# Kernel optimization log

Hardware: AMD Instinct MI355X
Metric: run time of the kernel (lower is better)

The kernel has to match this reference:

```python
import jax, jax.numpy as jnp
import numpy as np

DIM_RGB = 400
DIM_POSE = 400
HIDDEN = 512
LN_EPS = 1e-5


def setup_inputs() -> dict:
    key = jax.random.key(0)
    ks = jax.random.split(key, 12)
    B, S_R, S_P = 32, 2048, 2048
    scale_in = 1.0 / np.sqrt(DIM_RGB)
    scale_h = 1.0 / np.sqrt(HIDDEN)
    return {
        "rgb": jax.random.normal(ks[0], (B, S_R, DIM_RGB), jnp.float32),
        "pose": jax.random.normal(ks[1], (B, S_P, DIM_POSE), jnp.float32),
        "Wq": jax.random.normal(ks[2], (DIM_RGB, HIDDEN), jnp.float32) * scale_in,
        "bq": jnp.zeros((HIDDEN,), jnp.float32),
        "Wk": jax.random.normal(ks[3], (DIM_POSE, HIDDEN), jnp.float32) * scale_in,
        "bk": jnp.zeros((HIDDEN,), jnp.float32),
        "Wv": jax.random.normal(ks[4], (DIM_POSE, HIDDEN), jnp.float32) * scale_in,
        "bv": jnp.zeros((HIDDEN,), jnp.float32),
        "Wp": jax.random.normal(ks[5], (HIDDEN, DIM_RGB), jnp.float32) * scale_h,
        "bp": jnp.zeros((DIM_RGB,), jnp.float32),
        "ln_gamma": jnp.ones((DIM_RGB,), jnp.float32),
        "ln_beta": jnp.zeros((DIM_RGB,), jnp.float32),
        "gate": jnp.ones((1,), jnp.float32),
    }


def reference(rgb, pose, Wq, bq, Wk, bk, Wv, bv, Wp, bp, ln_gamma, ln_beta, gate):
    # q: [B,Sr,H], k/v: [B,Sp,H]
    q = jnp.einsum("bsd,dh->bsh", rgb, Wq) + bq
    k = jnp.einsum("bsd,dh->bsh", pose, Wk) + bk
    v = jnp.einsum("bsd,dh->bsh", pose, Wv) + bv
    scores = jnp.einsum("bqh,bkh->bqk", q, k) / jnp.sqrt(jnp.asarray(HIDDEN, q.dtype))
    attn = jax.nn.softmax(scores, axis=-1)  # [B,Sr,Sp]
    out = jnp.einsum("bqk,bkh->bqh", attn, v)
    proj = jnp.einsum("bqh,hd->bqd", out, Wp) + bp
    x = rgb + gate * proj  # gated residual, gate broadcasts from shape (1,)
    mu = jnp.mean(x, axis=-1, keepdims=True)
    var = jnp.mean(jnp.square(x - mu), axis=-1, keepdims=True)
    fused = (x - mu) * jax.lax.rsqrt(var + LN_EPS) * ln_gamma + ln_beta
    return fused
```

## Files before the change

### kernel.cpp

```cpp
#include <hip/hip_runtime.h>
#include <stdint.h>

typedef unsigned short u16;
typedef unsigned int u32;
typedef __bf16 bf16x8 __attribute__((ext_vector_type(8)));
typedef float f32x4 __attribute__((ext_vector_type(4)));

#define S_LEN 2048
#define BATCH 32
#define DIM 400
#define HID 512
#define KPAD 448
#define MROWS (BATCH * S_LEN)
#define NB_CHUNK 8
#define SCALE_QK 0.04419417382415922f

__device__ __forceinline__ u16 f2bf(float f) {
  u32 u = __float_as_uint(f);
  u = u + 0x7fffu + ((u >> 16) & 1u);
  return (u16)(u >> 16);
}
__device__ __forceinline__ float bf2f(u16 h) {
  return __uint_as_float(((u32)h) << 16);
}

__device__ __forceinline__ void async_cp16(const void* gp, const void* lp) {
  __builtin_amdgcn_global_load_lds(
      (const __attribute__((address_space(1))) void*)gp,
      (__attribute__((address_space(3))) void*)(uintptr_t)lp,
      16, 0, 0);
}

template<int BN>
__global__ __launch_bounds__(512, 2)
void gemm256(const u16* __restrict__ A, const u16* __restrict__ B,
             u16* __restrict__ C, const float* __restrict__ bias,
             int K, int lda, int ldb, int ldc, int Nreal, float scale,
             long sA, long sB, long sC, int mode)
{
  constexpr int NJ   = (BN == 256) ? 4 : 2;
  constexpr int COLW = (BN == 256) ? 64 : 32;
  constexpr int ASZ  = 16384;
  constexpr int BSZ  = (BN == 256) ? 16384 : 8192;
  __shared__ __align__(16) u16 SM[2 * ASZ + 2 * BSZ];

#define ABUF(i) (&SM[0] + (i) * ASZ)
#define BBUF(i) (&SM[0] + 2 * ASZ + (i) * BSZ)

  const int tid = threadIdx.x;
  const int lane = tid & 63;
  const int w = tid >> 6;
  const int wm = w >> 2, wn = w & 3;

  int mt, nt, bz;
  if (mode == 1) {
    const int lin = (int)blockIdx.x + ((int)blockIdx.y << 8);
    const int c = lin & 7, j = lin >> 3;
    mt = c * 32 + (j >> 1); nt = j & 1; bz = 0;
  } else if (mode == 2) {
    bz = blockIdx.x; mt = blockIdx.y; nt = blockIdx.z;
  } else if (mode == 3) {
    bz = blockIdx.x; mt = blockIdx.z; nt = blockIdx.y;
  } else {
    mt = blockIdx.x; nt = blockIdx.y; bz = blockIdx.z;
  }
  const long m0 = (long)mt * 256;
  const long n0 = (long)nt * BN;
  const u16* Ab = A + (long)bz * sA;
  const u16* Bb = B + (long)bz * sB;
  u16* Cb = C + (long)bz * sC;
  const int T = K >> 6;

  const int sr = tid >> 3, si = tid & 7;
  const u16 *gA[2][2], *gB[2][2];
#pragma unroll
  for (int h = 0; h < 2; h++)
#pragma unroll
    for (int j = 0; j < 2; j++) {
      const int Ra = h * 128 + sr + j * 64;
      const int ka = si ^ ((Ra >> 1) & 7);
      gA[h][j] = Ab + (m0 + Ra) * (long)lda + ka * 8;
      const int Rb = ((BN == 256) ? h * 128 : 0) + sr + j * 64;
      const int kb = si ^ ((Rb >> 1) & 7);
      gB[h][j] = Bb + (n0 + Rb) * (long)ldb + kb * 8;
    }

#define ISS(g0, g1, kt, lp) { async_cp16((g0) + (kt), (lp) + tid * 8); \
                              async_cp16((g1) + (kt), (lp) + 4096 + tid * 8); }

  if constexpr (BN == 256) {
    ISS(gB[0][0], gB[0][1], 0,  BBUF(0));
    ISS(gB[1][0], gB[1][1], 0,  BBUF(0) + 8192);
    ISS(gA[0][0], gA[0][1], 0,  ABUF(0));
    ISS(gA[1][0], gA[1][1], 0,  ABUF(0) + 8192);
    ISS(gB[0][0], gB[0][1], 64, BBUF(1));
    ISS(gB[1][0], gB[1][1], 64, BBUF(1) + 8192);
    asm volatile("s_waitcnt vmcnt(4)" ::: "memory");
  } else {
    ISS(gB[0][0], gB[0][1], 0,  BBUF(0));
    ISS(gA[0][0], gA[0][1], 0,  ABUF(0));
    ISS(gA[1][0], gA[1][1], 0,  ABUF(0) + 8192);
    ISS(gB[0][0], gB[0][1], 64, BBUF(1));
    asm volatile("s_waitcnt vmcnt(2)" ::: "memory");
  }
  asm volatile("s_barrier" ::: "memory");

  f32x4 acc[8][NJ] = {};
  const int l15 = lane & 15, l4 = lane >> 4;

#define LDA(dst, ig) { const int R_ = wm * 128 + (ig) * 16 + l15; \
    const int sw_ = (R_ >> 1) & 7; \
    dst[0] = *(const bf16x8*)&Asc[R_ * 64 + ((l4) ^ sw_) * 8]; \
    dst[1] = *(const bf16x8*)&Asc[R_ * 64 + ((4 + l4) ^ sw_) * 8]; }
#define LDB(dst, jg) { const int R_ = wn * COLW + (jg) * 16 + l15; \
    const int sw_ = (R_ >> 1) & 7; \
    dst[0] = *(const bf16x8*)&Bsc[R_ * 64 + ((l4) ^ sw_) * 8]; \
    dst[1] = *(const bf16x8*)&Bsc[R_ * 64 + ((4 + l4) ^ sw_) * 8]; }

  for (int t = 0; t < T; t++) {
    const int cur = t & 1, nxt = cur ^ 1;
    const u16* Asc = ABUF(cur);
    const u16* Bsc = BBUF(cur);
    const int kt1 = (t + 1) << 6, kt2 = (t + 2) << 6;
    bf16x8 afr[4][2], bfr[NJ][2];

    if (t + 1 < T) ISS(gA[0][0], gA[0][1], kt1, ABUF(nxt));
    LDB(bfr[0], 0); LDB(bfr[1], 1);
    if constexpr (BN == 256) { LDA(afr[0], 0); LDA(afr[1], 1); LDA(afr[2], 2); LDA(afr[3], 3); }
    else                     { LDA(afr[0], 0); LDA(afr[1], 1); }
    asm volatile("s_barrier" ::: "memory");
    __builtin_amdgcn_s_setprio(1);
#pragma unroll
    for (int ks = 0; ks < 2; ks++) {
      if constexpr (BN == 256) {
#pragma unroll
        for (int i = 0; i < 4; i++)
#pragma unroll
          for (int j = 0; j < 2; j++)
            acc[i][j] = __builtin_amdgcn_mfma_f32_16x16x32_bf16(afr[i][ks], bfr[j][ks], acc[i][j], 0, 0, 0);
      } else {
#pragma unroll
        for (int i = 0; i < 2; i++)
#pragma unroll
          for (int j = 0; j < 2; j++)
            acc[i][j] = __builtin_amdgcn_mfma_f32_16x16x32_bf16(afr[i][ks], bfr[j][ks], acc[i][j], 0, 0, 0);
      }
    }
    __builtin_amdgcn_s_setprio(0);
    asm volatile("s_barrier" ::: "memory");

    if (t + 1 < T) ISS(gA[1][0], gA[1][1], kt1, ABUF(nxt) + 8192);
    if constexpr (BN == 256) { LDB(bfr[2], 2); LDB(bfr[3], 3); }
    else                     { LDA(afr[2], 2); LDA(afr[3], 3); }
    asm volatile("s_barrier" ::: "memory");
    __builtin_amdgcn_s_setprio(1);
#pragma unroll
    for (int ks = 0; ks < 2; ks++) {
      if constexpr (BN == 256) {
#pragma unroll
        for (int i = 0; i < 4; i++)
#pragma unroll
          for (int j = 2; j < 4; j++)
            acc[i][j] = __builtin_amdgcn_mfma_f32_16x16x32_bf16(afr[i][ks], bfr[j][ks], acc[i][j], 0, 0, 0);
      } else {
#pragma unroll
        for (int i = 2; i < 4; i++)
#pragma unroll
          for (int j = 0; j < 2; j++)
            acc[i][j] = __builtin_amdgcn_mfma_f32_16x16x32_bf16(afr[i][ks], bfr[j][ks], acc[i][j], 0, 0, 0);
      }
    }
    __builtin_amdgcn_s_setprio(0);
    asm volatile("s_barrier" ::: "memory");

    if (t + 2 < T) ISS(gB[0][0], gB[0][1], kt2, BBUF(cur));
    if constexpr (BN == 256) { LDA(afr[0], 4); LDA(afr[1], 5); LDA(afr[2], 6); LDA(afr[3], 7); }
    else                     { LDA(afr[0], 4); LDA(afr[1], 5); }
    asm volatile("s_barrier" ::: "memory");
    __builtin_amdgcn_s_setprio(1);
#pragma unroll
    for (int ks = 0; ks < 2; ks++) {
      if constexpr (BN == 256) {
#pragma unroll
        for (int i = 0; i < 4; i++)
#pragma unroll
          for (int j = 0; j < 2; j++)
            acc[4 + i][j] = __builtin_amdgcn_mfma_f32_16x16x32_bf16(afr[i][ks], bfr[j][ks], acc[4 + i][j], 0, 0, 0);
      } else {
#pragma unroll
        for (int i = 0; i < 2; i++)
#pragma unroll
          for (int j = 0; j < 2; j++)
            acc[4 + i][j] = __builtin_amdgcn_mfma_f32_16x16x32_bf16(afr[i][ks], bfr[j][ks], acc[4 + i][j], 0, 0, 0);
      }
    }
    __builtin_amdgcn_s_setprio(0);
    asm volatile("s_barrier" ::: "memory");

    if constexpr (BN == 256) {
      if (t + 2 < T) ISS(gB[1][0], gB[1][1], kt2, BBUF(cur) + 8192);
    } else {
      LDA(afr[2], 6); LDA(afr[3], 7);
    }
    asm volatile("s_barrier" ::: "memory");
    __builtin_amdgcn_s_setprio(1);
#pragma unroll
    for (int ks = 0; ks < 2; ks++) {
      if constexpr (BN == 256) {
#pragma unroll
        for (int i = 0; i < 4; i++)
#pragma unroll
          for (int j = 2; j < 4; j++)
            acc[4 + i][j] = __builtin_amdgcn_mfma_f32_16x16x32_bf16(afr[i][ks], bfr[j][ks], acc[4 + i][j], 0, 0, 0);
      } else {
#pragma unroll
        for (int i = 2; i < 4; i++)
#pragma unroll
          for (int j = 0; j < 2; j++)
            acc[4 + i][j] = __builtin_amdgcn_mfma_f32_16x16x32_bf16(afr[i][ks], bfr[j][ks], acc[4 + i][j], 0, 0, 0);
      }
    }
    __builtin_amdgcn_s_setprio(0);
    if (t < T - 2) {
      if constexpr (BN == 256) asm volatile("s_waitcnt vmcnt(4)" ::: "memory");
      else                     asm volatile("s_waitcnt vmcnt(2)" ::: "memory");
    } else if (t == T - 2) {
      asm volatile("s_waitcnt vmcnt(0)" ::: "memory");
    }
    asm volatile("s_barrier" ::: "memory");
  }

  {
    u16* Cst = &SM[0];
    constexpr int RB = BN * 2;
#pragma unroll
    for (int j = 0; j < NJ; j++) {
      const int col = wn * COLW + j * 16 + l15;
      const int gcol = (int)n0 + col;
      const float bv = (bias && gcol < Nreal) ? bias[gcol] : 0.0f;
#pragma unroll
      for (int i = 0; i < 8; i++) {
#pragma unroll
        for (int r = 0; r < 4; r++) {
          const int row = wm * 128 + i * 16 + l4 * 4 + r;
          const int cb = (col * 2) ^ (((row >> 2) & 3) << 5);
          *(u16*)((char*)Cst + row * RB + cb) = f2bf(acc[i][j][r] * scale + bv);
        }
      }
    }
    __syncthreads();
    constexpr int CH = RB / 16;
    constexpr int NC = 256 * CH / 512;
#pragma unroll
    for (int i = 0; i < NC; i++) {
      const int chunk = tid + i * 512;
      const int row = chunk / CH;
      const int qb_ = (chunk % CH) * 16;
      const int swz = ((row >> 2) & 3) << 5;
      uint4 val = *(const uint4*)((const char*)Cst + row * RB + (qb_ ^ swz));
      const int col = (int)n0 + qb_ / 2;
      if (col < Nreal)
        *(uint4*)(Cb + (m0 + row) * (long)ldc + col) = val;
    }
  }
#undef ISS
#undef LDA
#undef LDB
#undef ABUF
#undef BBUF
}

__global__ __launch_bounds__(256)
void transpose_hs(const u16* __restrict__ v, u16* __restrict__ vT)
{
  __shared__ u16 tile[64][66];
  const int b = blockIdx.z;
  const long s0 = (long)blockIdx.x * 64;
  const long h0 = (long)blockIdx.y * 64;
  const u16* vb = v + (long)b * S_LEN * HID;
  u16* vTb = vT + (long)b * HID * S_LEN;
  const int t = threadIdx.x;
  const int rr = t >> 3;
  const int cs = (t & 7) * 8;
#pragma unroll
  for (int p = 0; p < 2; p++) {
    const int r = p * 32 + rr;
    uint4 d = *(const uint4*)(vb + (s0 + r) * HID + h0 + cs);
    const u16* ds = (const u16*)&d;
#pragma unroll
    for (int j = 0; j < 8; j++) tile[r][cs + j] = ds[j];
  }
  __syncthreads();
#pragma unroll
  for (int p = 0; p < 2; p++) {
    const int hc = p * 32 + rr;
    __align__(16) u16 tmp[8];
#pragma unroll
    for (int j = 0; j < 8; j++) tmp[j] = tile[cs + j][hc];
    *(uint4*)(vTb + (h0 + hc) * S_LEN + s0 + cs) = *(const uint4*)tmp;
  }
}

__global__ __launch_bounds__(256)
void softmax_rows(u16* __restrict__ sc)
{
  const int w = threadIdx.x >> 6, lane = threadIdx.x & 63;
  const long row = (long)blockIdx.x * 4 + w;
  u16* p = sc + row * (long)S_LEN;

  uint4 d[4];
#pragma unroll
  for (int k = 0; k < 4; k++) d[k] = *(const uint4*)(p + (k * 64 + lane) * 8);

  float x[32];
  float mx = -3.0e38f;
#pragma unroll
  for (int k = 0; k < 4; k++) {
    const u16* ds = (const u16*)&d[k];
#pragma unroll
    for (int j = 0; j < 8; j++) { x[k * 8 + j] = bf2f(ds[j]); mx = fmaxf(mx, x[k * 8 + j]); }
  }
#pragma unroll
  for (int o = 32; o > 0; o >>= 1) mx = fmaxf(mx, __shfl_xor(mx, o, 64));

  float s = 0.f;
#pragma unroll
  for (int e = 0; e < 32; e++) { x[e] = __expf(x[e] - mx); s += x[e]; }
#pragma unroll
  for (int o = 32; o > 0; o >>= 1) s += __shfl_xor(s, o, 64);
  const float inv = 1.0f / s;

#pragma unroll
  for (int k = 0; k < 4; k++) {
    __align__(16) u16 outv[8];
#pragma unroll
    for (int j = 0; j < 8; j++) outv[j] = f2bf(x[k * 8 + j] * inv);
    *(uint4*)(p + (k * 64 + lane) * 8) = *(const uint4*)outv;
  }
}

__global__ __launch_bounds__(256)
void fuse_ln(const float* __restrict__ rgb, const u16* __restrict__ proj,
             const float* __restrict__ gatep, const float* __restrict__ gamma,
             const float* __restrict__ beta, float* __restrict__ out)
{
  const int w = threadIdx.x >> 6, lane = threadIdx.x & 63;
  const long row = (long)blockIdx.x * 4 + w;
  const float g = gatep[0];
  const float* rp = rgb + row * DIM;
  const u16* pp = proj + row * DIM;
  float* op = out + row * DIM;
  const int c = lane * 8;
  const bool act = (lane < 50);

  float x[8];
  float s = 0.f, q = 0.f;
  if (act) {
    float4 r0 = *(const float4*)(rp + c);
    float4 r1 = *(const float4*)(rp + c + 4);
    uint4 pv = *(const uint4*)(pp + c);
    const u16* pb = (const u16*)&pv;
    float rr[8] = {r0.x, r0.y, r0.z, r0.w, r1.x, r1.y, r1.z, r1.w};
#pragma unroll
    for (int j = 0; j < 8; j++) {
      x[j] = rr[j] + g * bf2f(pb[j]);
      s += x[j]; q += x[j] * x[j];
    }
  }
#pragma unroll
  for (int o = 32; o > 0; o >>= 1) { s += __shfl_xor(s, o, 64); q += __shfl_xor(q, o, 64); }
  const float mean = s * (1.0f / DIM);
  const float var = q * (1.0f / DIM) - mean * mean;
  const float rstd = rsqrtf(var + 1e-5f);
  if (act) {
    float4 ga0 = *(const float4*)(gamma + c);
    float4 ga1 = *(const float4*)(gamma + c + 4);
    float4 be0 = *(const float4*)(beta + c);
    float4 be1 = *(const float4*)(beta + c + 4);
    float4 o0, o1;
    o0.x = (x[0] - mean) * rstd * ga0.x + be0.x;
    o0.y = (x[1] - mean) * rstd * ga0.y + be0.y;
    o0.z = (x[2] - mean) * rstd * ga0.z + be0.z;
    o0.w = (x[3] - mean) * rstd * ga0.w + be0.w;
    o1.x = (x[4] - mean) * rstd * ga1.x + be1.x;
    o1.y = (x[5] - mean) * rstd * ga1.y + be1.y;
    o1.z = (x[6] - mean) * rstd * ga1.z + be1.z;
    o1.w = (x[7] - mean) * rstd * ga1.w + be1.w;
    *(float4*)(op + c) = o0;
    *(float4*)(op + c + 4) = o1;
  }
}

__global__ __launch_bounds__(256)
void cvt_pad(const float* __restrict__ src, u16* __restrict__ dst)
{
  const long g = (long)blockIdx.x * 256 + threadIdx.x;
  const long row = g / 56;
  const int cs = (int)(g % 56) * 8;
  __align__(16) u16 o[8];
  if (cs + 8 <= DIM) {
    float4 r0 = *(const float4*)(src + row * DIM + cs);
    float4 r1 = *(const float4*)(src + row * DIM + cs + 4);
    float rr[8] = {r0.x, r0.y, r0.z, r0.w, r1.x, r1.y, r1.z, r1.w};
#pragma unroll
    for (int j = 0; j < 8; j++) o[j] = f2bf(rr[j]);
  } else {
#pragma unroll
    for (int j = 0; j < 8; j++) o[j] = 0;
  }
  *(uint4*)(dst + row * KPAD + cs) = *(const uint4*)o;
}

__global__ __launch_bounds__(256)
void cvt_wT(const float* __restrict__ W, u16* __restrict__ WT)
{
  const int g = blockIdx.x * 256 + threadIdx.x;
  const int n = g / KPAD;
  const int kc = g % KPAD;
  WT[g] = f2bf(kc < DIM ? W[(long)kc * HID + n] : 0.0f);
}

__global__ __launch_bounds__(256)
void cvt_wpT(const float* __restrict__ Wp, u16* __restrict__ WT)
{
  const int g = blockIdx.x * 256 + threadIdx.x;
  const int n = g / HID;
  const int kc = g % HID;
  WT[g] = f2bf(n < DIM ? Wp[(long)kc * DIM + n] : 0.0f);
}

extern "C" void kernel_launch(void* const* d_in, const int* in_sizes, int n_in,
                              void* d_out, int out_size, void* d_ws, size_t ws_size,
                              hipStream_t stream)
{
  const float* rgb  = (const float*)d_in[0];
  const float* pose = (const float*)d_in[1];
  const float* Wq   = (const float*)d_in[2];
  const float* bq   = (const float*)d_in[3];
  const float* Wk   = (const float*)d_in[4];
  const float* bk   = (const float*)d_in[5];
  const float* Wv   = (const float*)d_in[6];
  const float* bv   = (const float*)d_in[7];
  const float* Wp   = (const float*)d_in[8];
  const float* bp   = (const float*)d_in[9];
  const float* gam  = (const float*)d_in[10];
  const float* bet  = (const float*)d_in[11];
  const float* gate = (const float*)d_in[12];
  float* outp = (float*)d_out;
  char* ws = (char*)d_ws;

  const size_t SZ_PAD = (size_t)MROWS * KPAD * 2;
  const size_t SZ_SH  = (size_t)MROWS * HID * 2;
  u16* rgbp  = (u16*)(ws + 0);
  u16* posep = (u16*)(ws + SZ_PAD);
  u16* outb  = (u16*)(ws + 0);
  u16* projb = (u16*)(ws + SZ_SH);
  size_t off = 119537664;
  u16* wqT = (u16*)(ws + off); off += (size_t)HID * KPAD * 2;
  u16* wkT = (u16*)(ws + off); off += (size_t)HID * KPAD * 2;
  u16* wvT = (u16*)(ws + off); off += (size_t)HID * KPAD * 2;
  u16* wpT = (u16*)(ws + off); off += (size_t)HID * HID * 2;
  u16* qb  = (u16*)(ws + off); off += SZ_SH;
  u16* kb  = (u16*)(ws + off); off += SZ_SH;
  u16* vb  = (u16*)(ws + off);
  u16* scb = vb;
  off += SZ_SH;
  u16* vTb = (u16*)(ws + off); off += SZ_SH;

  cvt_pad<<<14336, 256, 0, stream>>>(rgb, rgbp);
  cvt_pad<<<14336, 256, 0, stream>>>(pose, posep);
  cvt_wT<<<896, 256, 0, stream>>>(Wq, wqT);
  cvt_wT<<<896, 256, 0, stream>>>(Wk, wkT);
  cvt_wT<<<896, 256, 0, stream>>>(Wv, wvT);
  cvt_wpT<<<1024, 256, 0, stream>>>(Wp, wpT);

  dim3 gQ(MROWS / 256, HID / 256, 1);
  gemm256<256><<<gQ, 512, 0, stream>>>(rgbp,  wqT, qb, bq, KPAD, KPAD, KPAD, HID, HID, 1.0f, 0, 0, 0, 1);
  gemm256<256><<<gQ, 512, 0, stream>>>(posep, wkT, kb, bk, KPAD, KPAD, KPAD, HID, HID, 1.0f, 0, 0, 0, 1);
  gemm256<256><<<gQ, 512, 0, stream>>>(posep, wvT, vb, bv, KPAD, KPAD, KPAD, HID, HID, 1.0f, 0, 0, 0, 1);

  dim3 gT(S_LEN / 64, HID / 64, BATCH);
  transpose_hs<<<gT, 256, 0, stream>>>(vb, vTb);

  const long sSH = (long)S_LEN * HID;
  const long sSS = (long)S_LEN * S_LEN;
  for (int c = 0; c < BATCH / NB_CHUNK; c++) {
    const size_t bo = (size_t)c * NB_CHUNK;
    dim3 g2(NB_CHUNK, S_LEN / 256, S_LEN / 256);
    gemm256<256><<<g2, 512, 0, stream>>>(qb + bo * sSH, kb + bo * sSH, scb, nullptr,
                                         HID, HID, HID, S_LEN, S_LEN, SCALE_QK, sSH, sSH, sSS, 2);
    softmax_rows<<<NB_CHUNK * S_LEN / 4, 256, 0, stream>>>(scb);
    dim3 g4(NB_CHUNK, HID / 128, S_LEN / 256);
    gemm256<128><<<g4, 512, 0, stream>>>(scb, vTb + bo * sSH, outb + bo * sSH, nullptr,
                                         S_LEN, S_LEN, S_LEN, HID, HID, 1.0f, sSS, sSH, sSH, 3);
  }

  gemm256<256><<<gQ, 512, 0, stream>>>(outb, wpT, projb, bp, HID, HID, HID, DIM, DIM, 1.0f, 0, 0, 0, 1);

  fuse_ln<<<MROWS / 4, 256, 0, stream>>>(rgb, projb, gate, gam, bet, outp);
}
```

Measured before the change: 940.8 us.

## Fuse softmax into QK and PV GEMM epilogues, write V transposed directly

Removes the standalone softmax kernel. The QK^T GEMM epilogue now writes exp(score*scale) without max subtraction, and the PV GEMM gets the row sums from an extra MFMA against a vector of ones, then divides in its epilogue. The V projection GEMM writes its output already transposed through LDS, which removes the separate transpose kernel and its round trip through memory. Skipping the max subtraction risks overflow for large scores and is only safe when scores stay small. The row-sum MFMA also adds matrix work to the PV GEMM.

```diff
diff --git a/kernel.cpp b/kernel.cpp
--- a/kernel.cpp
+++ b/kernel.cpp
@@ -31,7 +31,7 @@
       16, 0, 0);
 }
 
-template<int BN>
+template<int BN, int EPI, bool TRC>
 __global__ __launch_bounds__(512, 2)
 void gemm256(const u16* __restrict__ A, const u16* __restrict__ B,
              u16* __restrict__ C, const float* __restrict__ bias,
@@ -106,6 +106,10 @@
   asm volatile("s_barrier" ::: "memory");
 
   f32x4 acc[8][NJ] = {};
+  f32x4 acc_sum[8] = {};
+  bf16x8 onesf;
+#pragma unroll
+  for (int e = 0; e < 8; e++) onesf[e] = (__bf16)1.0f;
   const int l15 = lane & 15, l4 = lane >> 4;
 
 #define LDA(dst, ig) { const int R_ = wm * 128 + (ig) * 16 + l15; \
@@ -140,10 +144,13 @@
             acc[i][j] = __builtin_amdgcn_mfma_f32_16x16x32_bf16(afr[i][ks], bfr[j][ks], acc[i][j], 0, 0, 0);
       } else {
 #pragma unroll
-        for (int i = 0; i < 2; i++)
+        for (int i = 0; i < 2; i++) {
 #pragma unroll
           for (int j = 0; j < 2; j++)
             acc[i][j] = __builtin_amdgcn_mfma_f32_16x16x32_bf16(afr[i][ks], bfr[j][ks], acc[i][j], 0, 0, 0);
+          if constexpr (EPI == 2)
+            acc_sum[i] = __builtin_amdgcn_mfma_f32_16x16x32_bf16(afr[i][ks], onesf, acc_sum[i], 0, 0, 0);
+        }
       }
     }
     __builtin_amdgcn_s_setprio(0);
@@ -164,10 +171,13 @@
             acc[i][j] = __builtin_amdgcn_mfma_f32_16x16x32_bf16(afr[i][ks], bfr[j][ks], acc[i][j], 0, 0, 0);
       } else {
 #pragma unroll
-        for (int i = 2; i < 4; i++)
+        for (int i = 2; i < 4; i++) {
 #pragma unroll
           for (int j = 0; j < 2; j++)
             acc[i][j] = __builtin_amdgcn_mfma_f32_16x16x32_bf16(afr[i][ks], bfr[j][ks], acc[i][j], 0, 0, 0);
+          if constexpr (EPI == 2)
+            acc_sum[i] = __builtin_amdgcn_mfma_f32_16x16x32_bf16(afr[i][ks], onesf, acc_sum[i], 0, 0, 0);
+        }
       }
     }
     __builtin_amdgcn_s_setprio(0);
@@ -188,10 +198,13 @@
             acc[4 + i][j] = __builtin_amdgcn_mfma_f32_16x16x32_bf16(afr[i][ks], bfr[j][ks], acc[4 + i][j], 0, 0, 0);
       } else {
 #pragma unroll
-        for (int i = 0; i < 2; i++)
+        for (int i = 0; i < 2; i++) {
 #pragma unroll
           for (int j = 0; j < 2; j++)
             acc[4 + i][j] = __builtin_amdgcn_mfma_f32_16x16x32_bf16(afr[i][ks], bfr[j][ks], acc[4 + i][j], 0, 0, 0);
+          if constexpr (EPI == 2)
+            acc_sum[4 + i] = __builtin_amdgcn_mfma_f32_16x16x32_bf16(afr[i][ks], onesf, acc_sum[4 + i], 0, 0, 0);
+        }
       }
     }
     __builtin_amdgcn_s_setprio(0);
@@ -214,10 +227,13 @@
             acc[4 + i][j] = __builtin_amdgcn_mfma_f32_16x16x32_bf16(afr[i][ks], bfr[j][ks], acc[4 + i][j], 0, 0, 0);
       } else {
 #pragma unroll
-        for (int i = 2; i < 4; i++)
+        for (int i = 2; i < 4; i++) {
 #pragma unroll
           for (int j = 0; j < 2; j++)
             acc[4 + i][j] = __builtin_amdgcn_mfma_f32_16x16x32_bf16(afr[i][ks], bfr[j][ks], acc[4 + i][j], 0, 0, 0);
+          if constexpr (EPI == 2)
+            acc_sum[4 + i] = __builtin_amdgcn_mfma_f32_16x16x32_bf16(afr[i][ks], onesf, acc_sum[4 + i], 0, 0, 0);
+        }
       }
     }
     __builtin_amdgcn_s_setprio(0);
@@ -230,9 +246,44 @@
     asm volatile("s_barrier" ::: "memory");
   }
 
-  {
+  if constexpr (TRC) {
+    u16* Cst = &SM[0];
+#pragma unroll
+    for (int j = 0; j < NJ; j++) {
+      const int col = wn * COLW + j * 16 + l15;
+      const float bv = bias ? bias[(int)n0 + col] : 0.0f;
+#pragma unroll
+      for (int i = 0; i < 8; i++) {
+#pragma unroll
+        for (int r = 0; r < 4; r++) {
+          const int row = wm * 128 + i * 16 + l4 * 4 + r;
+          const int cb = (row * 2) ^ ((col & 7) << 5);
+          *(u16*)((char*)Cst + col * 512 + cb) = f2bf(acc[i][j][r] * scale + bv);
+        }
+      }
+    }
+    __syncthreads();
+    const long bb = m0 >> 11;
+    const int  s0 = (int)(m0 & 2047);
+    u16* vbase = C + bb * ((long)HID * (long)S_LEN);
+#pragma unroll
+    for (int it = 0; it < 16; it++) {
+      const int c2 = tid + it * 512;
+      const int col = c2 >> 5;
+      const int rs = c2 & 31;
+      uint4 val = *(const uint4*)((const char*)Cst + col * 512 + ((rs * 16) ^ ((col & 7) << 5)));
+      *(uint4*)(vbase + (long)((int)n0 + col) * S_LEN + s0 + rs * 8) = val;
+    }
+  } else {
     u16* Cst = &SM[0];
     constexpr int RB = BN * 2;
+    float invv[8][4];
+    if constexpr (EPI == 2) {
+#pragma unroll
+      for (int i = 0; i < 8; i++)
+#pragma unroll
+        for (int r = 0; r < 4; r++) invv[i][r] = 1.0f / acc_sum[i][r];
+    }
 #pragma unroll
     for (int j = 0; j < NJ; j++) {
       const int col = wn * COLW + j * 16 + l15;
@@ -244,7 +295,11 @@
         for (int r = 0; r < 4; r++) {
           const int row = wm * 128 + i * 16 + l4 * 4 + r;
           const int cb = (col * 2) ^ (((row >> 2) & 3) << 5);
-          *(u16*)((char*)Cst + row * RB + cb) = f2bf(acc[i][j][r] * scale + bv);
+          float v;
+          if constexpr (EPI == 1)      v = __expf(acc[i][j][r] * scale);
+          else if constexpr (EPI == 2) v = acc[i][j][r] * invv[i][r];
+          else                         v = acc[i][j][r] * scale + bv;
+          *(u16*)((char*)Cst + row * RB + cb) = f2bf(v);
         }
       }
     }
@@ -268,75 +323,6 @@
 #undef LDB
 #undef ABUF
 #undef BBUF
-}
-
-__global__ __launch_bounds__(256)
-void transpose_hs(const u16* __restrict__ v, u16* __restrict__ vT)
-{
-  __shared__ u16 tile[64][66];
-  const int b = blockIdx.z;
-  const long s0 = (long)blockIdx.x * 64;
-  const long h0 = (long)blockIdx.y * 64;
-  const u16* vb = v + (long)b * S_LEN * HID;
-  u16* vTb = vT + (long)b * HID * S_LEN;
-  const int t = threadIdx.x;
-  const int rr = t >> 3;
-  const int cs = (t & 7) * 8;
-#pragma unroll
-  for (int p = 0; p < 2; p++) {
-    const int r = p * 32 + rr;
-    uint4 d = *(const uint4*)(vb + (s0 + r) * HID + h0 + cs);
-    const u16* ds = (const u16*)&d;
-#pragma unroll
-    for (int j = 0; j < 8; j++) tile[r][cs + j] = ds[j];
-  }
-  __syncthreads();
-#pragma unroll
-  for (int p = 0; p < 2; p++) {
-    const int hc = p * 32 + rr;
-    __align__(16) u16 tmp[8];
-#pragma unroll
-    for (int j = 0; j < 8; j++) tmp[j] = tile[cs + j][hc];
-    *(uint4*)(vTb + (h0 + hc) * S_LEN + s0 + cs) = *(const uint4*)tmp;
-  }
-}
-
-__global__ __launch_bounds__(256)
-void softmax_rows(u16* __restrict__ sc)
-{
-  const int w = threadIdx.x >> 6, lane = threadIdx.x & 63;
-  const long row = (long)blockIdx.x * 4 + w;
-  u16* p = sc + row * (long)S_LEN;
-
-  uint4 d[4];
-#pragma unroll
-  for (int k = 0; k < 4; k++) d[k] = *(const uint4*)(p + (k * 64 + lane) * 8);
-
-  float x[32];
-  float mx = -3.0e38f;
-#pragma unroll
-  for (int k = 0; k < 4; k++) {
-    const u16* ds = (const u16*)&d[k];
-#pragma unroll
-    for (int j = 0; j < 8; j++) { x[k * 8 + j] = bf2f(ds[j]); mx = fmaxf(mx, x[k * 8 + j]); }
-  }
-#pragma unroll
-  for (int o = 32; o > 0; o >>= 1) mx = fmaxf(mx, __shfl_xor(mx, o, 64));
-
-  float s = 0.f;
-#pragma unroll
-  for (int e = 0; e < 32; e++) { x[e] = __expf(x[e] - mx); s += x[e]; }
-#pragma unroll
-  for (int o = 32; o > 0; o >>= 1) s += __shfl_xor(s, o, 64);
-  const float inv = 1.0f / s;
-
-#pragma unroll
-  for (int k = 0; k < 4; k++) {
-    __align__(16) u16 outv[8];
-#pragma unroll
-    for (int j = 0; j < 8; j++) outv[j] = f2bf(x[k * 8 + j] * inv);
-    *(uint4*)(p + (k * 64 + lane) * 8) = *(const uint4*)outv;
-  }
 }
 
 __global__ __launch_bounds__(256)
@@ -462,8 +448,7 @@
   u16* wpT = (u16*)(ws + off); off += (size_t)HID * HID * 2;
   u16* qb  = (u16*)(ws + off); off += SZ_SH;
   u16* kb  = (u16*)(ws + off); off += SZ_SH;
-  u16* vb  = (u16*)(ws + off);
-  u16* scb = vb;
+  u16* scb = (u16*)(ws + off);
   off += SZ_SH;
   u16* vTb = (u16*)(ws + off); off += SZ_SH;
 
@@ -475,27 +460,23 @@
   cvt_wpT<<<1024, 256, 0, stream>>>(Wp, wpT);
 
   dim3 gQ(MROWS / 256, HID / 256, 1);
-  gemm256<256><<<gQ, 512, 0, stream>>>(rgbp,  wqT, qb, bq, KPAD, KPAD, KPAD, HID, HID, 1.0f, 0, 0, 0, 1);
-  gemm256<256><<<gQ, 512, 0, stream>>>(posep, wkT, kb, bk, KPAD, KPAD, KPAD, HID, HID, 1.0f, 0, 0, 0, 1);
-  gemm256<256><<<gQ, 512, 0, stream>>>(posep, wvT, vb, bv, KPAD, KPAD, KPAD, HID, HID, 1.0f, 0, 0, 0, 1);
-
-  dim3 gT(S_LEN / 64, HID / 64, BATCH);
-  transpose_hs<<<gT, 256, 0, stream>>>(vb, vTb);
+  gemm256<256,0,false><<<gQ, 512, 0, stream>>>(rgbp,  wqT, qb,  bq, KPAD, KPAD, KPAD, HID, HID, 1.0f, 0, 0, 0, 1);
+  gemm256<256,0,false><<<gQ, 512, 0, stream>>>(posep, wkT, kb,  bk, KPAD, KPAD, KPAD, HID, HID, 1.0f, 0, 0, 0, 1);
+  gemm256<256,0,true ><<<gQ, 512, 0, stream>>>(posep, wvT, vTb, bv, KPAD, KPAD, KPAD, HID, HID, 1.0f, 0, 0, 0, 1);
 
   const long sSH = (long)S_LEN * HID;
   const long sSS = (long)S_LEN * S_LEN;
   for (int c = 0; c < BATCH / NB_CHUNK; c++) {
     const size_t bo = (size_t)c * NB_CHUNK;
     dim3 g2(NB_CHUNK, S_LEN / 256, S_LEN / 256);
-    gemm256<256><<<g2, 512, 0, stream>>>(qb + bo * sSH, kb + bo * sSH, scb, nullptr,
-                                         HID, HID, HID, S_LEN, S_LEN, SCALE_QK, sSH, sSH, sSS, 2);
-    softmax_rows<<<NB_CHUNK * S_LEN / 4, 256, 0, stream>>>(scb);
+    gemm256<256,1,false><<<g2, 512, 0, stream>>>(qb + bo * sSH, kb + bo * sSH, scb, nullptr,
+                                                 HID, HID, HID, S_LEN, S_LEN, SCALE_QK, sSH, sSH, sSS, 2);
     dim3 g4(NB_CHUNK, HID / 128, S_LEN / 256);
-    gemm256<128><<<g4, 512, 0, stream>>>(scb, vTb + bo * sSH, outb + bo * sSH, nullptr,
-                                         S_LEN, S_LEN, S_LEN, HID, HID, 1.0f, sSS, sSH, sSH, 3);
-  }
-
-  gemm256<256><<<gQ, 512, 0, stream>>>(outb, wpT, projb, bp, HID, HID, HID, DIM, DIM, 1.0f, 0, 0, 0, 1);
+    gemm256<128,2,false><<<g4, 512, 0, stream>>>(scb, vTb + bo * sSH, outb + bo * sSH, nullptr,
+                                                 S_LEN, S_LEN, S_LEN, HID, HID, 1.0f, sSS, sSH, sSH, 3);
+  }
+
+  gemm256<256,0,false><<<gQ, 512, 0, stream>>>(outb, wpT, projb, bp, HID, HID, HID, DIM, DIM, 1.0f, 0, 0, 0, 1);
 
   fuse_ln<<<MROWS / 4, 256, 0, stream>>>(rgb, projb, gate, gam, bet, outp);
 }
```

Measured after the change: 880.2 us. 1.07x faster.
